# Kernel optimization log

Hardware: AMD Instinct MI355X
Metric: run time of the kernel (lower is better)

The kernel has to match this reference:

```python
import jax, jax.numpy as jnp
import numpy as np

N_NODES = 100000
N_EDGES = 1600000
IN_DIM, EDGE_DIM, HID, HEADS = 2, 1, 64, 4
NEG_SLOPE = 0.2


def setup_inputs() -> dict:
    key = jax.random.key(0)
    ks = jax.random.split(key, 20)
    p = lambda k, shape: (jax.random.normal(k, shape, dtype=jnp.float32) * 0.1)
    inp = {
        "x": jax.random.normal(ks[0], (N_NODES, IN_DIM), dtype=jnp.float32),
        "edge_index": jax.random.randint(ks[1], (2, N_EDGES), 0, N_NODES, dtype=jnp.int32),
        "edge_attr": jax.random.uniform(ks[2], (N_EDGES, EDGE_DIM), dtype=jnp.float32),
        # conv1: heads=4, out=64, concat=True
        "W1": p(ks[3], (IN_DIM, HEADS * HID)),
        "We1": p(ks[4], (EDGE_DIM, HEADS * HID)),
        "as1": p(ks[5], (HEADS, HID)),
        "ad1": p(ks[6], (HEADS, HID)),
        "ae1": p(ks[7], (HEADS, HID)),
        "b1": jnp.zeros((HEADS * HID,), jnp.float32),
        # conv2: heads=1, out=64
        "W2": p(ks[8], (HEADS * HID, HID)),
        "We2": p(ks[9], (EDGE_DIM, HID)),
        "as2": p(ks[10], (1, HID)),
        "ad2": p(ks[11], (1, HID)),
        "ae2": p(ks[12], (1, HID)),
        "b2": jnp.zeros((HID,), jnp.float32),
        "Wr1": p(ks[13], (HID, HID)),
        "br1": jnp.zeros((HID,), jnp.float32),
        "Wr2": p(ks[14], (HID, 1)),
        "br2": jnp.zeros((1,), jnp.float32),
    }
    return inp


def gat_layer(x, src, dst, edge_attr, W, We, a_src, a_dst, a_edge, bias, heads, out_dim, n_nodes):
    """PyG GATConv (add_self_loops=False, concat=True, edge_dim set)."""
    h = (x @ W).reshape(n_nodes, heads, out_dim)          # [N,H,D]
    he = (edge_attr @ We).reshape(-1, heads, out_dim)     # [E,H,D]
    al_s = jnp.sum(h * a_src, axis=-1)                    # [N,H]
    al_d = jnp.sum(h * a_dst, axis=-1)                    # [N,H]
    al_e = jnp.sum(he * a_edge, axis=-1)                  # [E,H]
    logits = jax.nn.leaky_relu(al_s[src] + al_d[dst] + al_e, NEG_SLOPE)  # [E,H]
    # segment softmax over destination node
    m = jax.ops.segment_max(logits, dst, num_segments=n_nodes)
    p = jnp.exp(logits - m[dst])
    z = jax.ops.segment_sum(p, dst, num_segments=n_nodes)
    alpha = p / (z[dst] + 1e-16)                          # [E,H]
    msg = alpha[:, :, None] * h[src]                      # [E,H,D]
    out = jax.ops.segment_sum(msg, dst, num_segments=n_nodes)
    return out.reshape(n_nodes, heads * out_dim) + bias


def reference(x, edge_index, edge_attr, W1, We1, as1, ad1, ae1, b1,
              W2, We2, as2, ad2, ae2, b2, Wr1, br1, Wr2, br2):
    src, dst = edge_index[0], edge_index[1]
    n = x.shape[0]
    h = gat_layer(x, src, dst, edge_attr, W1, We1, as1, ad1, ae1, b1, HEADS, HID, n)
    h = gat_layer(h, src, dst, edge_attr, W2, We2, as2, ad2, ae2, b2, 1, HID, n)
    edge_emb = h[src] + h[dst]                             # [E,HID]
    hidden = jax.nn.relu(edge_emb @ Wr1 + br1)
    return (hidden @ Wr2 + br2).squeeze(-1)                # [E]
```

## Files before the change

kernel.cpp:

```cpp
#include <hip/hip_runtime.h>
#include <hip/hip_bf16.h>
#include <hip/hip_fp16.h>

#define NEG_SLOPE 0.2f
#define NBUCK_MAX 256
#define BCAP 12288
#define TILE 2048

typedef float v2f __attribute__((ext_vector_type(2)));

__device__ __forceinline__ float lrelu(float v) { return v >= 0.f ? v : NEG_SLOPE * v; }

__device__ __forceinline__ float wave_sum(float v) {
    for (int o = 32; o; o >>= 1) v += __shfl_down(v, o, 64);
    return v;
}

__device__ __forceinline__ void h8_to_f(const uint4 v, float* f) {
    float2 a = __half22float2(*(const __half2*)&v.x);
    float2 b = __half22float2(*(const __half2*)&v.y);
    float2 c = __half22float2(*(const __half2*)&v.z);
    float2 d = __half22float2(*(const __half2*)&v.w);
    f[0] = a.x; f[1] = a.y; f[2] = b.x; f[3] = b.y;
    f[4] = c.x; f[5] = c.y; f[6] = d.x; f[7] = d.y;
}

__device__ __forceinline__ void compute_ce1(const float* __restrict__ We1,
                                            const float* __restrict__ ae1,
                                            float* ce ) {
    int t = threadIdx.x;
    float p = wave_sum(We1[t] * ae1[t]);
    if ((t & 63) == 0) ce[t >> 6] = p;
    __syncthreads();
}

__device__ __forceinline__ float compute_ce2(const float* __restrict__ We2,
                                             const float* __restrict__ ae2,
                                             float* sh ) {
    int t = threadIdx.x;
    if (t < 64) {
        float p = wave_sum(We2[t] * ae2[t]);
        if (t == 0) sh[0] = p;
    }
    __syncthreads();
    return sh[0];
}

__global__ __launch_bounds__(256) void prep1_kernel(
    const float* __restrict__ x, const float* __restrict__ W1,
    const float* __restrict__ as1, const float* __restrict__ ad1,
    const float* __restrict__ W2, const float* __restrict__ b1,
    const float* __restrict__ Wr1, const float* __restrict__ b2,
    const float* __restrict__ as2, const float* __restrict__ ad2,
    const float* __restrict__ br1,
    float* __restrict__ rec, float* __restrict__ al_d1,
    int* __restrict__ bucket_cur, float* __restrict__ V, int N) {
    __shared__ float cs0[4], cs1[4], cd0[4], cd1[4];
    __shared__ float sV0[256], sV1[256], sc[64];
    int t = threadIdx.x;
    if (blockIdx.x == 0) bucket_cur[t] = t * BCAP;
    {
        float a = as1[t], d = ad1[t], u0 = W1[t], u1 = W1[256 + t];
        float p0 = wave_sum(u0 * a);
        float p1 = wave_sum(u1 * a);
        float q0 = wave_sum(u0 * d);
        float q1 = wave_sum(u1 * d);
        if ((t & 63) == 0) {
            int h = t >> 6;
            cs0[h] = p0; cs1[h] = p1; cd0[h] = q0; cd1[h] = q1;
        }
    }
    __syncthreads();
    int n = blockIdx.x * 256 + t;
    if (n < N) {
        float2 xs = ((const float2*)x)[n];
        float4 vs, vd;
        vs.x = xs.x * cs0[0] + xs.y * cs1[0];
        vs.y = xs.x * cs0[1] + xs.y * cs1[1];
        vs.z = xs.x * cs0[2] + xs.y * cs1[2];
        vs.w = xs.x * cs0[3] + xs.y * cs1[3];
        vd.x = xs.x * cd0[0] + xs.y * cd1[0];
        vd.y = xs.x * cd0[1] + xs.y * cd1[1];
        vd.z = xs.x * cd0[2] + xs.y * cd1[2];
        vd.w = xs.x * cd0[3] + xs.y * cd1[3];
        ((float4*)rec)[2 * n] = vs;
        ((float4*)rec)[2 * n + 1] = make_float4(xs.x, xs.y, 0.f, 0.f);
        ((float4*)al_d1)[n] = vd;
    }
    if (blockIdx.x == 0) {
        int h = t >> 6, j = t & 63;
        float v0 = 0.f, v1 = 0.f;
        for (int k = 0; k < 64; ++k) {
            float w2 = W2[(h * 64 + k) * 64 + j];
            v0 += W1[h * 64 + k] * w2;
            v1 += W1[256 + h * 64 + k] * w2;
        }
        sV0[t] = v0;
        sV1[t] = v1;
        if (t < 64) {
            float c = 0.f;
            for (int i = 0; i < 256; ++i) c += b1[i] * W2[i * 64 + t];
            sc[t] = c;
        }
        __syncthreads();
        float v0w = 0.f, v1w = 0.f;
        for (int k = 0; k < 64; ++k) {
            float wr = Wr1[k * 64 + j];
            v0w += sV0[h * 64 + k] * wr;
            v1w += sV1[h * 64 + k] * wr;
        }
        V[t] = v0w;
        V[256 + t] = v1w;
        if (t < 64) {
            float cw = 0.f, cb = 0.f;
            for (int k = 0; k < 64; ++k) {
                float wr = Wr1[k * 64 + t];
                cw += sc[k] * wr;
                cb += b2[k] * wr;
            }
            V[512 + t] = cw;
            V[576 + t] = cb;
            V[672 + t] = 2.f * cb + br1[t];
        }
        int lane = t & 63;
        float p0 = wave_sum(sV0[t] * as2[lane]);
        float p1 = wave_sum(sV1[t] * as2[lane]);
        float q0 = wave_sum(sV0[t] * ad2[lane]);
        float q1 = wave_sum(sV1[t] * ad2[lane]);
        if (lane == 0) {
            V[640 + h] = p0; V[644 + h] = p1; V[648 + h] = q0; V[652 + h] = q1;
        }
        if (t < 64) {
            float r0 = wave_sum(sc[t] * as2[t]);
            float r1 = wave_sum(sc[t] * ad2[t]);
            if (t == 0) { V[656] = r0; V[657] = r1; }
        }
    }
}

__global__ __launch_bounds__(256) void binA_kernel(
    const int* __restrict__ ei, const float* __restrict__ ea,
    int* __restrict__ bucket_cur, uint2* __restrict__ ebm, int E, int nbuck) {
    __shared__ int cnt[NBUCK_MAX];
    __shared__ int gbase[NBUCK_MAX];
    __shared__ int lofs[NBUCK_MAX];
    __shared__ int psum[NBUCK_MAX];
    __shared__ uint2 buf[TILE];
    __shared__ unsigned short bkt[TILE];
    int t = threadIdx.x;
    int e0 = blockIdx.x * TILE;
    int cntE = min(TILE, E - e0);
    for (int i = t; i < nbuck; i += 256) cnt[i] = 0;
    __syncthreads();
    uint2 rec[8];
    int rb[8], rr[8];
#pragma unroll
    for (int i = 0; i < 8; ++i) {
        int e = e0 + i * 256 + t;
        if (i * 256 + t < cntE) {
            int s = ei[e], d = ei[E + e];
            unsigned q = (unsigned)(ea[e] * 32767.f + 0.5f);
            q = min(q, 32767u);
            rec[i] = make_uint2((((unsigned)s) << 15) | q,
                                (unsigned)(((d & 511) << 21) | e));
            rb[i] = d >> 9;
            rr[i] = atomicAdd(&cnt[rb[i]], 1);
        } else {
            rb[i] = -1;
        }
    }
    __syncthreads();
    int v = (t < nbuck) ? cnt[t] : 0;
    psum[t] = v;
    __syncthreads();
    for (int o = 1; o < 256; o <<= 1) {
        int a = (t >= o) ? psum[t - o] : 0;
        __syncthreads();
        psum[t] += a;
        __syncthreads();
    }
    if (t < nbuck) {
        lofs[t] = psum[t] - v;
        if (v) gbase[t] = atomicAdd(&bucket_cur[t], v);
    }
    __syncthreads();
#pragma unroll
    for (int i = 0; i < 8; ++i) {
        if (rb[i] >= 0) {
            int p = lofs[rb[i]] + rr[i];
            buf[p] = rec[i];
            bkt[p] = (unsigned short)rb[i];
        }
    }
    __syncthreads();
    for (int p = t; p < cntE; p += 256) {
        int b = bkt[p];
        ebm[gbase[b] + (p - lofs[b])] = buf[p];
    }
}

__global__ __launch_bounds__(256) void binB_kernel(
    const uint2* __restrict__ ebm, const int* __restrict__ bucket_cur,
    int* __restrict__ deg, int* __restrict__ offs,
    unsigned* __restrict__ csr_se, int N) {
    __shared__ int lcnt[512];
    __shared__ int lofs[512];
    __shared__ int lcur[512];
    int b = blockIdx.x;
    int n0 = b << 9;
    int t = threadIdx.x;
    lcnt[t] = 0; lcnt[t + 256] = 0;
    __syncthreads();
    int bstart = b * BCAP;
    int bend = bucket_cur[b];
    for (int p = bstart + t; p < bend; p += 256)
        atomicAdd(&lcnt[ebm[p].y >> 21], 1);
    __syncthreads();
    int a0 = lcnt[2 * t], a1 = lcnt[2 * t + 1];
    __shared__ int psum[256];
    psum[t] = a0 + a1;
    __syncthreads();
    for (int o = 1; o < 256; o <<= 1) {
        int a = (t >= o) ? psum[t - o] : 0;
        __syncthreads();
        psum[t] += a;
        __syncthreads();
    }
    int excl = psum[t] - (a0 + a1);
    lofs[2 * t] = excl;
    lofs[2 * t + 1] = excl + a0;
    lcur[2 * t] = bstart + excl;
    lcur[2 * t + 1] = bstart + excl + a0;
    __syncthreads();
    for (int i = t; i < 512; i += 256) {
        int n = n0 + i;
        if (n < N) {
            deg[n] = lcnt[i];
            offs[n] = bstart + lofs[i] + lcnt[i];
        }
    }
    for (int p = bstart + t; p < bend; p += 256) {
        uint2 m = ebm[p];
        int pos = atomicAdd(&lcur[m.y >> 21], 1);
        csr_se[pos] = m.x;
    }
}

__global__ __launch_bounds__(256) void aggX_kernel(
    const unsigned* __restrict__ csr_se, const int* __restrict__ offs,
    const int* __restrict__ deg,
    const float* __restrict__ rec, const float* __restrict__ al_d1,
    const float* __restrict__ We1, const float* __restrict__ ae1,
    const float* __restrict__ V,
    float2* __restrict__ XA, float* __restrict__ al_s2, float* __restrict__ al_d2,
    int N) {
    __shared__ float ce[4];
    __shared__ float sS[18];
    if (threadIdx.x < 18) sS[threadIdx.x] = V[640 + threadIdx.x];
    compute_ce1(We1, ae1, ce);
    int t = blockIdx.x * 256 + threadIdx.x;
    int n = t >> 2, h = t & 3;
    if (n >= N) return;
    int dc = deg[n];
    int start = offs[n] - dc;
    float ald = al_d1[4 * n + h];
    float ceh = ce[h] * (1.f / 32767.f);
    float z = 0.f, X0 = 0.f, X1 = 0.f;
    int j = 0;
    for (; j + 2 <= dc; j += 2) {
        unsigned w0 = csr_se[start + j];
        unsigned w1 = csr_se[start + j + 1];
        int s0 = w0 >> 15, s1 = w1 >> 15;
        const float* rb0 = rec + (size_t)8 * s0;
        const float* rb1 = rec + (size_t)8 * s1;
        float als0 = rb0[h];
        float als1 = rb1[h];
        float2 xs0 = *(const float2*)(rb0 + 4);
        float2 xs1 = *(const float2*)(rb1 + 4);
        float e0 = __expf(lrelu(als0 + ald + (float)(w0 & 32767u) * ceh));
        float e1 = __expf(lrelu(als1 + ald + (float)(w1 & 32767u) * ceh));
        z += e0 + e1;
        X0 += e0 * xs0.x + e1 * xs1.x;
        X1 += e0 * xs0.y + e1 * xs1.y;
    }
    if (j < dc) {
        unsigned w = csr_se[start + j];
        int s = w >> 15;
        const float* rb = rec + (size_t)8 * s;
        float als = rb[h];
        float2 xs = *(const float2*)(rb + 4);
        float ex = __expf(lrelu(als + ald + (float)(w & 32767u) * ceh));
        z += ex;
        X0 += ex * xs.x;
        X1 += ex * xs.y;
    }
    float inv = 1.f / (z + 1e-16f);
    float xa0 = X0 * inv, xa1 = X1 * inv;
    XA[(size_t)4 * n + h] = make_float2(xa0, xa1);
    float ps = xa0 * sS[h] + xa1 * sS[4 + h];
    float pd = xa0 * sS[8 + h] + xa1 * sS[12 + h];
    ps += __shfl_xor(ps, 1, 64); ps += __shfl_xor(ps, 2, 64);
    pd += __shfl_xor(pd, 1, 64); pd += __shfl_xor(pd, 2, 64);
    if (h == 0) {
        al_s2[n] = sS[16] + ps;
        al_d2[n] = sS[17] + pd;
    }
}

__global__ __launch_bounds__(256) void msg2y_kernel(
    const unsigned* __restrict__ csr_se, const int* __restrict__ offs,
    const int* __restrict__ deg,
    const float* __restrict__ al_d2,
    const float* __restrict__ We2, const float* __restrict__ ae2,
    const float* __restrict__ V,
    const float2* __restrict__ XA,
    uint4* __restrict__ Yh, float* __restrict__ w0n, int N) {
    __shared__ float sh[1];
    float ce2 = compute_ce2(We2, ae2, sh) * (1.f / 32767.f);
    float s16 = V[656];
    float ss0 = V[640], ss1 = V[641], ss2 = V[642], ss3 = V[643];
    float ss4 = V[644], ss5 = V[645], ss6 = V[646], ss7 = V[647];
    int t = blockIdx.x * 256 + threadIdx.x;
    int n = t >> 2, q = t & 3;
    if (n >= N) return;
    int dc = deg[n];
    int start = offs[n] - dc;
    float ald = al_d2[n];
    const float4* xa4 = (const float4*)XA;
    float y0 = 0.f, y1 = 0.f, y2 = 0.f, y3 = 0.f;
    float y4 = 0.f, y5 = 0.f, y6 = 0.f, y7 = 0.f;
    float z = 0.f;
    int j = q;
    for (; j + 4 < dc; j += 8) {
        unsigned wA = csr_se[start + j];
        unsigned wB = csr_se[start + j + 4];
        int sA = wA >> 15, sB = wB >> 15;
        float4 a0 = xa4[(size_t)sA * 2];
        float4 a1 = xa4[(size_t)sA * 2 + 1];
        float4 b0 = xa4[(size_t)sB * 2];
        float4 b1 = xa4[(size_t)sB * 2 + 1];
        float alsA = s16 + a0.x * ss0 + a0.y * ss4 + a0.z * ss1 + a0.w * ss5
                         + a1.x * ss2 + a1.y * ss6 + a1.z * ss3 + a1.w * ss7;
        float alsB = s16 + b0.x * ss0 + b0.y * ss4 + b0.z * ss1 + b0.w * ss5
                         + b1.x * ss2 + b1.y * ss6 + b1.z * ss3 + b1.w * ss7;
        float exA = __expf(lrelu(alsA + ald + (float)(wA & 32767u) * ce2));
        float exB = __expf(lrelu(alsB + ald + (float)(wB & 32767u) * ce2));
        z += exA + exB;
        y0 += exA * a0.x + exB * b0.x;
        y1 += exA * a0.y + exB * b0.y;
        y2 += exA * a0.z + exB * b0.z;
        y3 += exA * a0.w + exB * b0.w;
        y4 += exA * a1.x + exB * b1.x;
        y5 += exA * a1.y + exB * b1.y;
        y6 += exA * a1.z + exB * b1.z;
        y7 += exA * a1.w + exB * b1.w;
    }
    if (j < dc) {
        unsigned w = csr_se[start + j];
        int s = w >> 15;
        float4 a0 = xa4[(size_t)s * 2];
        float4 a1 = xa4[(size_t)s * 2 + 1];
        float als = s16 + a0.x * ss0 + a0.y * ss4 + a0.z * ss1 + a0.w * ss5
                        + a1.x * ss2 + a1.y * ss6 + a1.z * ss3 + a1.w * ss7;
        float ex = __expf(lrelu(als + ald + (float)(w & 32767u) * ce2));
        z += ex;
        y0 += ex * a0.x; y1 += ex * a0.y; y2 += ex * a0.z; y3 += ex * a0.w;
        y4 += ex * a1.x; y5 += ex * a1.y; y6 += ex * a1.z; y7 += ex * a1.w;
    }
    y0 += __shfl_xor(y0, 1, 64); y0 += __shfl_xor(y0, 2, 64);
    y1 += __shfl_xor(y1, 1, 64); y1 += __shfl_xor(y1, 2, 64);
    y2 += __shfl_xor(y2, 1, 64); y2 += __shfl_xor(y2, 2, 64);
    y3 += __shfl_xor(y3, 1, 64); y3 += __shfl_xor(y3, 2, 64);
    y4 += __shfl_xor(y4, 1, 64); y4 += __shfl_xor(y4, 2, 64);
    y5 += __shfl_xor(y5, 1, 64); y5 += __shfl_xor(y5, 2, 64);
    y6 += __shfl_xor(y6, 1, 64); y6 += __shfl_xor(y6, 2, 64);
    y7 += __shfl_xor(y7, 1, 64); y7 += __shfl_xor(y7, 2, 64);
    z += __shfl_xor(z, 1, 64); z += __shfl_xor(z, 2, 64);
    if (q == 0) {
        float inv = 1.f / (z + 1e-16f);
        __half2 p0 = __floats2half2_rn(y0 * inv, y1 * inv);
        __half2 p1 = __floats2half2_rn(y2 * inv, y3 * inv);
        __half2 p2 = __floats2half2_rn(y4 * inv, y5 * inv);
        __half2 p3 = __floats2half2_rn(y6 * inv, y7 * inv);
        uint4 o;
        o.x = *(unsigned*)&p0; o.y = *(unsigned*)&p1;
        o.z = *(unsigned*)&p2; o.w = *(unsigned*)&p3;
        Yh[n] = o;
        w0n[n] = z * inv;
    }
}

__global__ __launch_bounds__(256) void edge_kernel(
    const int* __restrict__ ei,
    const uint4* __restrict__ Yh, const float* __restrict__ w0n,
    const float* __restrict__ V,
    const float* __restrict__ Wr2,
    const float* __restrict__ br2, float* __restrict__ out, int E) {
    int e = blockIdx.x * 256 + threadIdx.x;
    if (e >= E) return;
    int s = ei[e], d = ei[E + e];
    uint4 ys = Yh[s], yd = Yh[d];
    float w0 = w0n[s] + w0n[d];
    float fs[8], fd[8], tt[8];
    h8_to_f(ys, fs);
    h8_to_f(yd, fd);
#pragma unroll
    for (int i = 0; i < 8; ++i) tt[i] = fs[i] + fd[i];
    v2f acc = {0.f, 0.f};
    v2f w0v = {w0, w0};
#pragma unroll
    for (int k = 0; k < 64; k += 2) {
        v2f g = w0v * (*(const v2f*)(V + 512 + k));
        g += *(const v2f*)(V + 672 + k);
        g += (v2f){tt[0], tt[0]} * (*(const v2f*)(V + k));
        g += (v2f){tt[1], tt[1]} * (*(const v2f*)(V + 256 + k));
        g += (v2f){tt[2], tt[2]} * (*(const v2f*)(V + 64 + k));
        g += (v2f){tt[3], tt[3]} * (*(const v2f*)(V + 320 + k));
        g += (v2f){tt[4], tt[4]} * (*(const v2f*)(V + 128 + k));
        g += (v2f){tt[5], tt[5]} * (*(const v2f*)(V + 384 + k));
        g += (v2f){tt[6], tt[6]} * (*(const v2f*)(V + 192 + k));
        g += (v2f){tt[7], tt[7]} * (*(const v2f*)(V + 448 + k));
        g = __builtin_elementwise_max(g, (v2f){0.f, 0.f});
        acc += g * (*(const v2f*)(Wr2 + k));
    }
    out[e] = acc.x + acc.y + br2[0];
}

extern "C" void kernel_launch(void* const* d_in, const int* in_sizes, int n_in,
                              void* d_out, int out_size, void* d_ws, size_t ws_size,
                              hipStream_t stream) {
    const float* x    = (const float*)d_in[0];
    const int*   ei   = (const int*)d_in[1];
    const float* ea   = (const float*)d_in[2];
    const float* W1   = (const float*)d_in[3];
    const float* We1  = (const float*)d_in[4];
    const float* as1  = (const float*)d_in[5];
    const float* ad1  = (const float*)d_in[6];
    const float* ae1  = (const float*)d_in[7];
    const float* b1   = (const float*)d_in[8];
    const float* W2   = (const float*)d_in[9];
    const float* We2  = (const float*)d_in[10];
    const float* as2  = (const float*)d_in[11];
    const float* ad2  = (const float*)d_in[12];
    const float* ae2  = (const float*)d_in[13];
    const float* b2   = (const float*)d_in[14];
    const float* Wr1  = (const float*)d_in[15];
    const float* br1  = (const float*)d_in[16];
    const float* Wr2  = (const float*)d_in[17];
    const float* br2  = (const float*)d_in[18];
    float* out = (float*)d_out;

    const int N = in_sizes[0] / 2;
    const int E = in_sizes[2];
    const int nbuck = (N + 511) >> 9;
    const size_t capE = (size_t)nbuck * BCAP;

    float* ws = (float*)d_ws;
    float*    rec   = ws;
    float*    al_d1 = rec + (size_t)N * 8;
    float*    al_s2 = al_d1 + (size_t)N * 4;
    float*    al_d2 = al_s2 + N;
    float2*   XA    = (float2*)((((uintptr_t)(al_d2 + N)) + 31) & ~(uintptr_t)31);
    float*    V     = (float*)((((uintptr_t)(XA + (size_t)N * 4)) + 15) & ~(uintptr_t)15);
    int*      deg   = (int*)(V + 768);
    int*      offs  = deg + N;
    int*      bucket_cur  = offs + N;
    uint4*    Yh    = (uint4*)((((uintptr_t)(bucket_cur + 256)) + 15) & ~(uintptr_t)15);
    float*    w0n   = (float*)(Yh + N);
    uint2*    ebm   = (uint2*)((((uintptr_t)(w0n + N)) + 15) & ~(uintptr_t)15);
    unsigned* csr_se = (unsigned*)(ebm + capE);

    const int nb = (N + 255) / 256;

    prep1_kernel<<<nb, 256, 0, stream>>>(x, W1, as1, ad1, W2, b1, Wr1, b2, as2, ad2,
                                         br1, rec, al_d1, bucket_cur, V, N);
    binA_kernel<<<(E + TILE - 1) / TILE, 256, 0, stream>>>(ei, ea, bucket_cur, ebm,
                                                           E, nbuck);
    binB_kernel<<<nbuck, 256, 0, stream>>>(ebm, bucket_cur, deg, offs, csr_se, N);
    aggX_kernel<<<(4 * N + 255) / 256, 256, 0, stream>>>(csr_se, offs, deg,
                                                         rec, al_d1, We1, ae1, V,
                                                         XA, al_s2, al_d2, N);
    msg2y_kernel<<<(4 * N + 255) / 256, 256, 0, stream>>>(csr_se, offs, deg,
                                                          al_d2, We2, ae2, V, XA,
                                                          Yh, w0n, N);
    edge_kernel<<<(E + 255) / 256, 256, 0, stream>>>(ei, Yh, w0n, V, Wr2, br2,
                                                     out, E);
}
```

Before: 223.2 us.

## Replace CSR build with per-bucket LDS atomic aggregation for both GAT layers

Drops the binB counting-sort kernel that built a CSR by destination. The two aggregation kernels now read the bucketed edge list directly, one 512-thread block per 512-node bucket, and accumulate the softmax numerators and denominators with shared-memory float atomics. This removes a kernel launch and a full pass that wrote and reread the CSR. In exchange it adds heavy LDS atomic traffic (12 or 9 atomics per edge) and makes the summation order nondeterministic. al_d2 is now computed inside msg2y2 instead of being stored by the first aggregation kernel.

```diff
diff --git a/kernel.cpp b/kernel.cpp
--- a/kernel.cpp
+++ b/kernel.cpp
@@ -23,27 +23,6 @@
     float2 d = __half22float2(*(const __half2*)&v.w);
     f[0] = a.x; f[1] = a.y; f[2] = b.x; f[3] = b.y;
     f[4] = c.x; f[5] = c.y; f[6] = d.x; f[7] = d.y;
-}
-
-__device__ __forceinline__ void compute_ce1(const float* __restrict__ We1,
-                                            const float* __restrict__ ae1,
-                                            float* ce ) {
-    int t = threadIdx.x;
-    float p = wave_sum(We1[t] * ae1[t]);
-    if ((t & 63) == 0) ce[t >> 6] = p;
-    __syncthreads();
-}
-
-__device__ __forceinline__ float compute_ce2(const float* __restrict__ We2,
-                                             const float* __restrict__ ae2,
-                                             float* sh ) {
-    int t = threadIdx.x;
-    if (t < 64) {
-        float p = wave_sum(We2[t] * ae2[t]);
-        if (t == 0) sh[0] = p;
-    }
-    __syncthreads();
-    return sh[0];
 }
 
 __global__ __launch_bounds__(256) void prep1_kernel(
@@ -199,189 +178,121 @@
     }
 }
 
-__global__ __launch_bounds__(256) void binB_kernel(
+__global__ __launch_bounds__(512) void aggX2_kernel(
     const uint2* __restrict__ ebm, const int* __restrict__ bucket_cur,
-    int* __restrict__ deg, int* __restrict__ offs,
-    unsigned* __restrict__ csr_se, int N) {
-    __shared__ int lcnt[512];
-    __shared__ int lofs[512];
-    __shared__ int lcur[512];
-    int b = blockIdx.x;
-    int n0 = b << 9;
-    int t = threadIdx.x;
-    lcnt[t] = 0; lcnt[t + 256] = 0;
-    __syncthreads();
-    int bstart = b * BCAP;
-    int bend = bucket_cur[b];
-    for (int p = bstart + t; p < bend; p += 256)
-        atomicAdd(&lcnt[ebm[p].y >> 21], 1);
-    __syncthreads();
-    int a0 = lcnt[2 * t], a1 = lcnt[2 * t + 1];
-    __shared__ int psum[256];
-    psum[t] = a0 + a1;
-    __syncthreads();
-    for (int o = 1; o < 256; o <<= 1) {
-        int a = (t >= o) ? psum[t - o] : 0;
-        __syncthreads();
-        psum[t] += a;
-        __syncthreads();
-    }
-    int excl = psum[t] - (a0 + a1);
-    lofs[2 * t] = excl;
-    lofs[2 * t + 1] = excl + a0;
-    lcur[2 * t] = bstart + excl;
-    lcur[2 * t + 1] = bstart + excl + a0;
-    __syncthreads();
-    for (int i = t; i < 512; i += 256) {
-        int n = n0 + i;
-        if (n < N) {
-            deg[n] = lcnt[i];
-            offs[n] = bstart + lofs[i] + lcnt[i];
-        }
-    }
-    for (int p = bstart + t; p < bend; p += 256) {
-        uint2 m = ebm[p];
-        int pos = atomicAdd(&lcur[m.y >> 21], 1);
-        csr_se[pos] = m.x;
-    }
-}
-
-__global__ __launch_bounds__(256) void aggX_kernel(
-    const unsigned* __restrict__ csr_se, const int* __restrict__ offs,
-    const int* __restrict__ deg,
     const float* __restrict__ rec, const float* __restrict__ al_d1,
     const float* __restrict__ We1, const float* __restrict__ ae1,
-    const float* __restrict__ V,
-    float2* __restrict__ XA, float* __restrict__ al_s2, float* __restrict__ al_d2,
-    int N) {
+    float2* __restrict__ XA, int N) {
     __shared__ float ce[4];
-    __shared__ float sS[18];
-    if (threadIdx.x < 18) sS[threadIdx.x] = V[640 + threadIdx.x];
-    compute_ce1(We1, ae1, ce);
-    int t = blockIdx.x * 256 + threadIdx.x;
-    int n = t >> 2, h = t & 3;
-    if (n >= N) return;
-    int dc = deg[n];
-    int start = offs[n] - dc;
-    float ald = al_d1[4 * n + h];
-    float ceh = ce[h] * (1.f / 32767.f);
-    float z = 0.f, X0 = 0.f, X1 = 0.f;
-    int j = 0;
-    for (; j + 2 <= dc; j += 2) {
-        unsigned w0 = csr_se[start + j];
-        unsigned w1 = csr_se[start + j + 1];
-        int s0 = w0 >> 15, s1 = w1 >> 15;
-        const float* rb0 = rec + (size_t)8 * s0;
-        const float* rb1 = rec + (size_t)8 * s1;
-        float als0 = rb0[h];
-        float als1 = rb1[h];
-        float2 xs0 = *(const float2*)(rb0 + 4);
-        float2 xs1 = *(const float2*)(rb1 + 4);
-        float e0 = __expf(lrelu(als0 + ald + (float)(w0 & 32767u) * ceh));
-        float e1 = __expf(lrelu(als1 + ald + (float)(w1 & 32767u) * ceh));
-        z += e0 + e1;
-        X0 += e0 * xs0.x + e1 * xs1.x;
-        X1 += e0 * xs0.y + e1 * xs1.y;
-    }
-    if (j < dc) {
-        unsigned w = csr_se[start + j];
-        int s = w >> 15;
-        const float* rb = rec + (size_t)8 * s;
-        float als = rb[h];
-        float2 xs = *(const float2*)(rb + 4);
-        float ex = __expf(lrelu(als + ald + (float)(w & 32767u) * ceh));
-        z += ex;
-        X0 += ex * xs.x;
-        X1 += ex * xs.y;
-    }
-    float inv = 1.f / (z + 1e-16f);
-    float xa0 = X0 * inv, xa1 = X1 * inv;
-    XA[(size_t)4 * n + h] = make_float2(xa0, xa1);
-    float ps = xa0 * sS[h] + xa1 * sS[4 + h];
-    float pd = xa0 * sS[8 + h] + xa1 * sS[12 + h];
-    ps += __shfl_xor(ps, 1, 64); ps += __shfl_xor(ps, 2, 64);
-    pd += __shfl_xor(pd, 1, 64); pd += __shfl_xor(pd, 2, 64);
-    if (h == 0) {
-        al_s2[n] = sS[16] + ps;
-        al_d2[n] = sS[17] + pd;
-    }
-}
-
-__global__ __launch_bounds__(256) void msg2y_kernel(
-    const unsigned* __restrict__ csr_se, const int* __restrict__ offs,
-    const int* __restrict__ deg,
-    const float* __restrict__ al_d2,
+    __shared__ float acc[512 * 12];
+    __shared__ float4 sald[512];
+    int t = threadIdx.x;
+    int b = blockIdx.x, n0 = b << 9;
+    if (t < 256) {
+        float p = wave_sum(We1[t] * ae1[t]);
+        if ((t & 63) == 0) ce[t >> 6] = p;
+    }
+#pragma unroll
+    for (int i = 0; i < 12; ++i) acc[t * 12 + i] = 0.f;
+    int n = n0 + t;
+    sald[t] = (n < N) ? ((const float4*)al_d1)[n] : make_float4(0.f, 0.f, 0.f, 0.f);
+    __syncthreads();
+    float c0 = ce[0] * (1.f / 32767.f), c1 = ce[1] * (1.f / 32767.f);
+    float c2 = ce[2] * (1.f / 32767.f), c3 = ce[3] * (1.f / 32767.f);
+    int bstart = b * BCAP, bend = bucket_cur[b];
+    for (int p = bstart + t; p < bend; p += 512) {
+        uint2 m = ebm[p];
+        int src = m.x >> 15;
+        float q = (float)(m.x & 32767u);
+        int dl = m.y >> 21;
+        const float4* rp = (const float4*)(rec + (size_t)8 * src);
+        float4 als = rp[0];
+        float4 xs = rp[1];
+        float4 ad = sald[dl];
+        float e0 = __expf(lrelu(als.x + ad.x + q * c0));
+        float e1 = __expf(lrelu(als.y + ad.y + q * c1));
+        float e2 = __expf(lrelu(als.z + ad.z + q * c2));
+        float e3 = __expf(lrelu(als.w + ad.w + q * c3));
+        float* a = acc + dl * 12;
+        atomicAdd(a + 0, e0);       atomicAdd(a + 1, e1);
+        atomicAdd(a + 2, e2);       atomicAdd(a + 3, e3);
+        atomicAdd(a + 4, e0 * xs.x); atomicAdd(a + 5, e1 * xs.x);
+        atomicAdd(a + 6, e2 * xs.x); atomicAdd(a + 7, e3 * xs.x);
+        atomicAdd(a + 8, e0 * xs.y); atomicAdd(a + 9, e1 * xs.y);
+        atomicAdd(a + 10, e2 * xs.y); atomicAdd(a + 11, e3 * xs.y);
+    }
+    __syncthreads();
+    if (n < N) {
+        float* a = acc + t * 12;
+        float i0 = 1.f / (a[0] + 1e-16f);
+        float i1 = 1.f / (a[1] + 1e-16f);
+        float i2 = 1.f / (a[2] + 1e-16f);
+        float i3 = 1.f / (a[3] + 1e-16f);
+        ((float4*)XA)[2 * n]     = make_float4(a[4] * i0, a[8] * i0, a[5] * i1, a[9] * i1);
+        ((float4*)XA)[2 * n + 1] = make_float4(a[6] * i2, a[10] * i2, a[7] * i3, a[11] * i3);
+    }
+}
+
+__global__ __launch_bounds__(512) void msg2y2_kernel(
+    const uint2* __restrict__ ebm, const int* __restrict__ bucket_cur,
     const float* __restrict__ We2, const float* __restrict__ ae2,
-    const float* __restrict__ V,
-    const float2* __restrict__ XA,
+    const float* __restrict__ V, const float2* __restrict__ XA,
     uint4* __restrict__ Yh, float* __restrict__ w0n, int N) {
     __shared__ float sh[1];
-    float ce2 = compute_ce2(We2, ae2, sh) * (1.f / 32767.f);
-    float s16 = V[656];
+    __shared__ float acc[512 * 9];
+    __shared__ float sald[512];
+    int t = threadIdx.x;
+    int b = blockIdx.x, n0 = b << 9;
+    if (t < 64) {
+        float p = wave_sum(We2[t] * ae2[t]);
+        if (t == 0) sh[0] = p;
+    }
+    float s16 = V[656], s17 = V[657];
     float ss0 = V[640], ss1 = V[641], ss2 = V[642], ss3 = V[643];
     float ss4 = V[644], ss5 = V[645], ss6 = V[646], ss7 = V[647];
-    int t = blockIdx.x * 256 + threadIdx.x;
-    int n = t >> 2, q = t & 3;
-    if (n >= N) return;
-    int dc = deg[n];
-    int start = offs[n] - dc;
-    float ald = al_d2[n];
+    float sd0 = V[648], sd1 = V[649], sd2 = V[650], sd3 = V[651];
+    float sd4 = V[652], sd5 = V[653], sd6 = V[654], sd7 = V[655];
+#pragma unroll
+    for (int i = 0; i < 9; ++i) acc[t * 9 + i] = 0.f;
+    int n = n0 + t;
     const float4* xa4 = (const float4*)XA;
-    float y0 = 0.f, y1 = 0.f, y2 = 0.f, y3 = 0.f;
-    float y4 = 0.f, y5 = 0.f, y6 = 0.f, y7 = 0.f;
-    float z = 0.f;
-    int j = q;
-    for (; j + 4 < dc; j += 8) {
-        unsigned wA = csr_se[start + j];
-        unsigned wB = csr_se[start + j + 4];
-        int sA = wA >> 15, sB = wB >> 15;
-        float4 a0 = xa4[(size_t)sA * 2];
-        float4 a1 = xa4[(size_t)sA * 2 + 1];
-        float4 b0 = xa4[(size_t)sB * 2];
-        float4 b1 = xa4[(size_t)sB * 2 + 1];
-        float alsA = s16 + a0.x * ss0 + a0.y * ss4 + a0.z * ss1 + a0.w * ss5
-                         + a1.x * ss2 + a1.y * ss6 + a1.z * ss3 + a1.w * ss7;
-        float alsB = s16 + b0.x * ss0 + b0.y * ss4 + b0.z * ss1 + b0.w * ss5
-                         + b1.x * ss2 + b1.y * ss6 + b1.z * ss3 + b1.w * ss7;
-        float exA = __expf(lrelu(alsA + ald + (float)(wA & 32767u) * ce2));
-        float exB = __expf(lrelu(alsB + ald + (float)(wB & 32767u) * ce2));
-        z += exA + exB;
-        y0 += exA * a0.x + exB * b0.x;
-        y1 += exA * a0.y + exB * b0.y;
-        y2 += exA * a0.z + exB * b0.z;
-        y3 += exA * a0.w + exB * b0.w;
-        y4 += exA * a1.x + exB * b1.x;
-        y5 += exA * a1.y + exB * b1.y;
-        y6 += exA * a1.z + exB * b1.z;
-        y7 += exA * a1.w + exB * b1.w;
-    }
-    if (j < dc) {
-        unsigned w = csr_se[start + j];
-        int s = w >> 15;
-        float4 a0 = xa4[(size_t)s * 2];
-        float4 a1 = xa4[(size_t)s * 2 + 1];
+    if (n < N) {
+        float4 a0 = xa4[(size_t)2 * n];
+        float4 a1 = xa4[(size_t)2 * n + 1];
+        sald[t] = s17 + a0.x * sd0 + a0.y * sd4 + a0.z * sd1 + a0.w * sd5
+                      + a1.x * sd2 + a1.y * sd6 + a1.z * sd3 + a1.w * sd7;
+    } else {
+        sald[t] = 0.f;
+    }
+    __syncthreads();
+    float ce2 = sh[0] * (1.f / 32767.f);
+    int bstart = b * BCAP, bend = bucket_cur[b];
+    for (int p = bstart + t; p < bend; p += 512) {
+        uint2 m = ebm[p];
+        int src = m.x >> 15;
+        float q = (float)(m.x & 32767u);
+        int dl = m.y >> 21;
+        float4 a0 = xa4[(size_t)2 * src];
+        float4 a1 = xa4[(size_t)2 * src + 1];
         float als = s16 + a0.x * ss0 + a0.y * ss4 + a0.z * ss1 + a0.w * ss5
                         + a1.x * ss2 + a1.y * ss6 + a1.z * ss3 + a1.w * ss7;
-        float ex = __expf(lrelu(als + ald + (float)(w & 32767u) * ce2));
-        z += ex;
-        y0 += ex * a0.x; y1 += ex * a0.y; y2 += ex * a0.z; y3 += ex * a0.w;
-        y4 += ex * a1.x; y5 += ex * a1.y; y6 += ex * a1.z; y7 += ex * a1.w;
-    }
-    y0 += __shfl_xor(y0, 1, 64); y0 += __shfl_xor(y0, 2, 64);
-    y1 += __shfl_xor(y1, 1, 64); y1 += __shfl_xor(y1, 2, 64);
-    y2 += __shfl_xor(y2, 1, 64); y2 += __shfl_xor(y2, 2, 64);
-    y3 += __shfl_xor(y3, 1, 64); y3 += __shfl_xor(y3, 2, 64);
-    y4 += __shfl_xor(y4, 1, 64); y4 += __shfl_xor(y4, 2, 64);
-    y5 += __shfl_xor(y5, 1, 64); y5 += __shfl_xor(y5, 2, 64);
-    y6 += __shfl_xor(y6, 1, 64); y6 += __shfl_xor(y6, 2, 64);
-    y7 += __shfl_xor(y7, 1, 64); y7 += __shfl_xor(y7, 2, 64);
-    z += __shfl_xor(z, 1, 64); z += __shfl_xor(z, 2, 64);
-    if (q == 0) {
+        float ex = __expf(lrelu(als + sald[dl] + q * ce2));
+        float* a = acc + dl * 9;
+        atomicAdd(a + 0, ex);
+        atomicAdd(a + 1, ex * a0.x); atomicAdd(a + 2, ex * a0.y);
+        atomicAdd(a + 3, ex * a0.z); atomicAdd(a + 4, ex * a0.w);
+        atomicAdd(a + 5, ex * a1.x); atomicAdd(a + 6, ex * a1.y);
+        atomicAdd(a + 7, ex * a1.z); atomicAdd(a + 8, ex * a1.w);
+    }
+    __syncthreads();
+    if (n < N) {
+        float* a = acc + t * 9;
+        float z = a[0];
         float inv = 1.f / (z + 1e-16f);
-        __half2 p0 = __floats2half2_rn(y0 * inv, y1 * inv);
-        __half2 p1 = __floats2half2_rn(y2 * inv, y3 * inv);
-        __half2 p2 = __floats2half2_rn(y4 * inv, y5 * inv);
-        __half2 p3 = __floats2half2_rn(y6 * inv, y7 * inv);
+        __half2 p0 = __floats2half2_rn(a[1] * inv, a[2] * inv);
+        __half2 p1 = __floats2half2_rn(a[3] * inv, a[4] * inv);
+        __half2 p2 = __floats2half2_rn(a[5] * inv, a[6] * inv);
+        __half2 p3 = __floats2half2_rn(a[7] * inv, a[8] * inv);
         uint4 o;
         o.x = *(unsigned*)&p0; o.y = *(unsigned*)&p1;
         o.z = *(unsigned*)&p2; o.w = *(unsigned*)&p3;
@@ -458,17 +369,12 @@
     float* ws = (float*)d_ws;
     float*    rec   = ws;
     float*    al_d1 = rec + (size_t)N * 8;
-    float*    al_s2 = al_d1 + (size_t)N * 4;
-    float*    al_d2 = al_s2 + N;
-    float2*   XA    = (float2*)((((uintptr_t)(al_d2 + N)) + 31) & ~(uintptr_t)31);
+    float2*   XA    = (float2*)((((uintptr_t)(al_d1 + (size_t)N * 4)) + 31) & ~(uintptr_t)31);
     float*    V     = (float*)((((uintptr_t)(XA + (size_t)N * 4)) + 15) & ~(uintptr_t)15);
-    int*      deg   = (int*)(V + 768);
-    int*      offs  = deg + N;
-    int*      bucket_cur  = offs + N;
+    int*      bucket_cur = (int*)(V + 768);
     uint4*    Yh    = (uint4*)((((uintptr_t)(bucket_cur + 256)) + 15) & ~(uintptr_t)15);
     float*    w0n   = (float*)(Yh + N);
     uint2*    ebm   = (uint2*)((((uintptr_t)(w0n + N)) + 15) & ~(uintptr_t)15);
-    unsigned* csr_se = (unsigned*)(ebm + capE);
 
     const int nb = (N + 255) / 256;
 
@@ -476,13 +382,10 @@
                                          br1, rec, al_d1, bucket_cur, V, N);
     binA_kernel<<<(E + TILE - 1) / TILE, 256, 0, stream>>>(ei, ea, bucket_cur, ebm,
                                                            E, nbuck);
-    binB_kernel<<<nbuck, 256, 0, stream>>>(ebm, bucket_cur, deg, offs, csr_se, N);
-    aggX_kernel<<<(4 * N + 255) / 256, 256, 0, stream>>>(csr_se, offs, deg,
-                                                         rec, al_d1, We1, ae1, V,
-                                                         XA, al_s2, al_d2, N);
-    msg2y_kernel<<<(4 * N + 255) / 256, 256, 0, stream>>>(csr_se, offs, deg,
-                                                          al_d2, We2, ae2, V, XA,
-                                                          Yh, w0n, N);
+    aggX2_kernel<<<nbuck, 512, 0, stream>>>(ebm, bucket_cur, rec, al_d1,
+                                            We1, ae1, XA, N);
+    msg2y2_kernel<<<nbuck, 512, 0, stream>>>(ebm, bucket_cur, We2, ae2, V, XA,
+                                             Yh, w0n, N);
     edge_kernel<<<(E + 255) / 256, 256, 0, stream>>>(ei, Yh, w0n, V, Wr2, br2,
                                                      out, E);
 }
```

Measured after the change: 400.1 us. 1.79x slower.

## Count degrees with global atomics in binning and split edges across lanes in aggX

Applied to the files above, without the earlier changes.

Node in-degrees are now counted with global atomics in binA (deg is zeroed in prep1), so binB no longer makes a separate counting pass over its bucket before the scan. aggX changes its work split: each of the four lanes per node now handles a strided quarter of the edges and computes all four heads, loading the full float4 records. Partial sums are then combined with cross-lane shuffles. This removes one pass over ebm and cuts per-head redundant gathers, at the cost of 1.6M global atomics and more registers and shuffles in aggX.

```diff
diff --git a/kernel.cpp b/kernel.cpp
--- a/kernel.cpp
+++ b/kernel.cpp
@@ -53,7 +53,7 @@
     const float* __restrict__ Wr1, const float* __restrict__ b2,
     const float* __restrict__ as2, const float* __restrict__ ad2,
     const float* __restrict__ br1,
-    float* __restrict__ rec, float* __restrict__ al_d1,
+    float* __restrict__ rec, float* __restrict__ al_d1, int* __restrict__ deg,
     int* __restrict__ bucket_cur, float* __restrict__ V, int N) {
     __shared__ float cs0[4], cs1[4], cd0[4], cd1[4];
     __shared__ float sV0[256], sV1[256], sc[64];
@@ -73,6 +73,7 @@
     __syncthreads();
     int n = blockIdx.x * 256 + t;
     if (n < N) {
+        deg[n] = 0;
         float2 xs = ((const float2*)x)[n];
         float4 vs, vd;
         vs.x = xs.x * cs0[0] + xs.y * cs1[0];
@@ -140,7 +141,8 @@
 
 __global__ __launch_bounds__(256) void binA_kernel(
     const int* __restrict__ ei, const float* __restrict__ ea,
-    int* __restrict__ bucket_cur, uint2* __restrict__ ebm, int E, int nbuck) {
+    int* __restrict__ bucket_cur, int* __restrict__ deg,
+    uint2* __restrict__ ebm, int E, int nbuck) {
     __shared__ int cnt[NBUCK_MAX];
     __shared__ int gbase[NBUCK_MAX];
     __shared__ int lofs[NBUCK_MAX];
@@ -165,6 +167,7 @@
                                 (unsigned)(((d & 511) << 21) | e));
             rb[i] = d >> 9;
             rr[i] = atomicAdd(&cnt[rb[i]], 1);
+            atomicAdd(&deg[d], 1);
         } else {
             rb[i] = -1;
         }
@@ -201,23 +204,16 @@
 
 __global__ __launch_bounds__(256) void binB_kernel(
     const uint2* __restrict__ ebm, const int* __restrict__ bucket_cur,
-    int* __restrict__ deg, int* __restrict__ offs,
+    const int* __restrict__ deg, int* __restrict__ offs,
     unsigned* __restrict__ csr_se, int N) {
-    __shared__ int lcnt[512];
-    __shared__ int lofs[512];
     __shared__ int lcur[512];
+    __shared__ int psum[256];
     int b = blockIdx.x;
     int n0 = b << 9;
     int t = threadIdx.x;
-    lcnt[t] = 0; lcnt[t + 256] = 0;
-    __syncthreads();
-    int bstart = b * BCAP;
-    int bend = bucket_cur[b];
-    for (int p = bstart + t; p < bend; p += 256)
-        atomicAdd(&lcnt[ebm[p].y >> 21], 1);
-    __syncthreads();
-    int a0 = lcnt[2 * t], a1 = lcnt[2 * t + 1];
-    __shared__ int psum[256];
+    int na = n0 + 2 * t, nb2 = na + 1;
+    int a0 = (na < N) ? deg[na] : 0;
+    int a1 = (nb2 < N) ? deg[nb2] : 0;
     psum[t] = a0 + a1;
     __syncthreads();
     for (int o = 1; o < 256; o <<= 1) {
@@ -227,18 +223,13 @@
         __syncthreads();
     }
     int excl = psum[t] - (a0 + a1);
-    lofs[2 * t] = excl;
-    lofs[2 * t + 1] = excl + a0;
+    int bstart = b * BCAP;
     lcur[2 * t] = bstart + excl;
     lcur[2 * t + 1] = bstart + excl + a0;
-    __syncthreads();
-    for (int i = t; i < 512; i += 256) {
-        int n = n0 + i;
-        if (n < N) {
-            deg[n] = lcnt[i];
-            offs[n] = bstart + lofs[i] + lcnt[i];
-        }
-    }
+    if (na < N) offs[na] = bstart + excl + a0;
+    if (nb2 < N) offs[nb2] = bstart + excl + a0 + a1;
+    __syncthreads();
+    int bend = bucket_cur[b];
     for (int p = bstart + t; p < bend; p += 256) {
         uint2 m = ebm[p];
         int pos = atomicAdd(&lcur[m.y >> 21], 1);
@@ -259,49 +250,85 @@
     if (threadIdx.x < 18) sS[threadIdx.x] = V[640 + threadIdx.x];
     compute_ce1(We1, ae1, ce);
     int t = blockIdx.x * 256 + threadIdx.x;
-    int n = t >> 2, h = t & 3;
+    int n = t >> 2, q = t & 3;
     if (n >= N) return;
     int dc = deg[n];
     int start = offs[n] - dc;
-    float ald = al_d1[4 * n + h];
-    float ceh = ce[h] * (1.f / 32767.f);
-    float z = 0.f, X0 = 0.f, X1 = 0.f;
-    int j = 0;
-    for (; j + 2 <= dc; j += 2) {
-        unsigned w0 = csr_se[start + j];
-        unsigned w1 = csr_se[start + j + 1];
-        int s0 = w0 >> 15, s1 = w1 >> 15;
-        const float* rb0 = rec + (size_t)8 * s0;
-        const float* rb1 = rec + (size_t)8 * s1;
-        float als0 = rb0[h];
-        float als1 = rb1[h];
-        float2 xs0 = *(const float2*)(rb0 + 4);
-        float2 xs1 = *(const float2*)(rb1 + 4);
-        float e0 = __expf(lrelu(als0 + ald + (float)(w0 & 32767u) * ceh));
-        float e1 = __expf(lrelu(als1 + ald + (float)(w1 & 32767u) * ceh));
-        z += e0 + e1;
-        X0 += e0 * xs0.x + e1 * xs1.x;
-        X1 += e0 * xs0.y + e1 * xs1.y;
+    float4 ad = ((const float4*)al_d1)[n];
+    float c0 = ce[0] * (1.f / 32767.f), c1 = ce[1] * (1.f / 32767.f);
+    float c2 = ce[2] * (1.f / 32767.f), c3 = ce[3] * (1.f / 32767.f);
+    const float4* r4 = (const float4*)rec;
+    float z0 = 0.f, z1 = 0.f, z2 = 0.f, z3 = 0.f;
+    float a0 = 0.f, a1 = 0.f, a2 = 0.f, a3 = 0.f;
+    float b0 = 0.f, b1 = 0.f, b2 = 0.f, b3 = 0.f;
+    int j = q;
+    for (; j + 4 < dc; j += 8) {
+        unsigned wA = csr_se[start + j];
+        unsigned wB = csr_se[start + j + 4];
+        int sA = wA >> 15, sB = wB >> 15;
+        float qA = (float)(wA & 32767u), qB = (float)(wB & 32767u);
+        float4 alsA = r4[(size_t)2 * sA];
+        float4 xsA  = r4[(size_t)2 * sA + 1];
+        float4 alsB = r4[(size_t)2 * sB];
+        float4 xsB  = r4[(size_t)2 * sB + 1];
+        float eA0 = __expf(lrelu(alsA.x + ad.x + qA * c0));
+        float eA1 = __expf(lrelu(alsA.y + ad.y + qA * c1));
+        float eA2 = __expf(lrelu(alsA.z + ad.z + qA * c2));
+        float eA3 = __expf(lrelu(alsA.w + ad.w + qA * c3));
+        float eB0 = __expf(lrelu(alsB.x + ad.x + qB * c0));
+        float eB1 = __expf(lrelu(alsB.y + ad.y + qB * c1));
+        float eB2 = __expf(lrelu(alsB.z + ad.z + qB * c2));
+        float eB3 = __expf(lrelu(alsB.w + ad.w + qB * c3));
+        z0 += eA0 + eB0; z1 += eA1 + eB1; z2 += eA2 + eB2; z3 += eA3 + eB3;
+        a0 += eA0 * xsA.x + eB0 * xsB.x;
+        a1 += eA1 * xsA.x + eB1 * xsB.x;
+        a2 += eA2 * xsA.x + eB2 * xsB.x;
+        a3 += eA3 * xsA.x + eB3 * xsB.x;
+        b0 += eA0 * xsA.y + eB0 * xsB.y;
+        b1 += eA1 * xsA.y + eB1 * xsB.y;
+        b2 += eA2 * xsA.y + eB2 * xsB.y;
+        b3 += eA3 * xsA.y + eB3 * xsB.y;
     }
     if (j < dc) {
         unsigned w = csr_se[start + j];
         int s = w >> 15;
-        const float* rb = rec + (size_t)8 * s;
-        float als = rb[h];
-        float2 xs = *(const float2*)(rb + 4);
-        float ex = __expf(lrelu(als + ald + (float)(w & 32767u) * ceh));
-        z += ex;
-        X0 += ex * xs.x;
-        X1 += ex * xs.y;
-    }
-    float inv = 1.f / (z + 1e-16f);
-    float xa0 = X0 * inv, xa1 = X1 * inv;
-    XA[(size_t)4 * n + h] = make_float2(xa0, xa1);
-    float ps = xa0 * sS[h] + xa1 * sS[4 + h];
-    float pd = xa0 * sS[8 + h] + xa1 * sS[12 + h];
-    ps += __shfl_xor(ps, 1, 64); ps += __shfl_xor(ps, 2, 64);
-    pd += __shfl_xor(pd, 1, 64); pd += __shfl_xor(pd, 2, 64);
-    if (h == 0) {
+        float qv = (float)(w & 32767u);
+        float4 als = r4[(size_t)2 * s];
+        float4 xs  = r4[(size_t)2 * s + 1];
+        float e0 = __expf(lrelu(als.x + ad.x + qv * c0));
+        float e1 = __expf(lrelu(als.y + ad.y + qv * c1));
+        float e2 = __expf(lrelu(als.z + ad.z + qv * c2));
+        float e3 = __expf(lrelu(als.w + ad.w + qv * c3));
+        z0 += e0; z1 += e1; z2 += e2; z3 += e3;
+        a0 += e0 * xs.x; a1 += e1 * xs.x; a2 += e2 * xs.x; a3 += e3 * xs.x;
+        b0 += e0 * xs.y; b1 += e1 * xs.y; b2 += e2 * xs.y; b3 += e3 * xs.y;
+    }
+    z0 += __shfl_xor(z0, 1, 64); z0 += __shfl_xor(z0, 2, 64);
+    z1 += __shfl_xor(z1, 1, 64); z1 += __shfl_xor(z1, 2, 64);
+    z2 += __shfl_xor(z2, 1, 64); z2 += __shfl_xor(z2, 2, 64);
+    z3 += __shfl_xor(z3, 1, 64); z3 += __shfl_xor(z3, 2, 64);
+    a0 += __shfl_xor(a0, 1, 64); a0 += __shfl_xor(a0, 2, 64);
+    a1 += __shfl_xor(a1, 1, 64); a1 += __shfl_xor(a1, 2, 64);
+    a2 += __shfl_xor(a2, 1, 64); a2 += __shfl_xor(a2, 2, 64);
+    a3 += __shfl_xor(a3, 1, 64); a3 += __shfl_xor(a3, 2, 64);
+    b0 += __shfl_xor(b0, 1, 64); b0 += __shfl_xor(b0, 2, 64);
+    b1 += __shfl_xor(b1, 1, 64); b1 += __shfl_xor(b1, 2, 64);
+    b2 += __shfl_xor(b2, 1, 64); b2 += __shfl_xor(b2, 2, 64);
+    b3 += __shfl_xor(b3, 1, 64); b3 += __shfl_xor(b3, 2, 64);
+    float i0 = 1.f / (z0 + 1e-16f);
+    float i1 = 1.f / (z1 + 1e-16f);
+    float i2 = 1.f / (z2 + 1e-16f);
+    float i3 = 1.f / (z3 + 1e-16f);
+    float xa0h = (q == 0) ? a0 * i0 : (q == 1) ? a1 * i1 : (q == 2) ? a2 * i2 : a3 * i3;
+    float xa1h = (q == 0) ? b0 * i0 : (q == 1) ? b1 * i1 : (q == 2) ? b2 * i2 : b3 * i3;
+    XA[(size_t)4 * n + q] = make_float2(xa0h, xa1h);
+    if (q == 0) {
+        float x00 = a0 * i0, x01 = a1 * i1, x02 = a2 * i2, x03 = a3 * i3;
+        float x10 = b0 * i0, x11 = b1 * i1, x12 = b2 * i2, x13 = b3 * i3;
+        float ps = x00 * sS[0] + x01 * sS[1] + x02 * sS[2] + x03 * sS[3]
+                 + x10 * sS[4] + x11 * sS[5] + x12 * sS[6] + x13 * sS[7];
+        float pd = x00 * sS[8] + x01 * sS[9] + x02 * sS[10] + x03 * sS[11]
+                 + x10 * sS[12] + x11 * sS[13] + x12 * sS[14] + x13 * sS[15];
         al_s2[n] = sS[16] + ps;
         al_d2[n] = sS[17] + pd;
     }
@@ -473,9 +500,9 @@
     const int nb = (N + 255) / 256;
 
     prep1_kernel<<<nb, 256, 0, stream>>>(x, W1, as1, ad1, W2, b1, Wr1, b2, as2, ad2,
-                                         br1, rec, al_d1, bucket_cur, V, N);
-    binA_kernel<<<(E + TILE - 1) / TILE, 256, 0, stream>>>(ei, ea, bucket_cur, ebm,
-                                                           E, nbuck);
+                                         br1, rec, al_d1, deg, bucket_cur, V, N);
+    binA_kernel<<<(E + TILE - 1) / TILE, 256, 0, stream>>>(ei, ea, bucket_cur, deg,
+                                                           ebm, E, nbuck);
     binB_kernel<<<nbuck, 256, 0, stream>>>(ebm, bucket_cur, deg, offs, csr_se, N);
     aggX_kernel<<<(4 * N + 255) / 256, 256, 0, stream>>>(csr_se, offs, deg,
                                                          rec, al_d1, We1, ae1, V,
```

New measurement: 278.0 us. +24.5%, slower.
